# Kernel tuning notes

Measured on AMD Instinct MI355X. Metric: run time of the kernel, lower is better.

Reference implementation:

```python
import jax, jax.numpy as jnp
import numpy as np

L, R, H, E = 2, 3, 512, 32768

def setup_inputs() -> dict:
    key = jax.random.key(0)
    ks = jax.random.split(key, 8)
    s = 1.0 / np.sqrt(H)  # keep activations sane
    return {
        "v_repr": jax.random.normal(ks[0], (E, H), jnp.float32),
        "r_repr": jax.random.normal(ks[1], (E, H), jnp.float32),
        "ent_roles": jax.random.randint(ks[2], (E,), 0, R),
        "W": jax.random.normal(ks[3], (L, R, H, H), jnp.float32) * s,
        "W_b": jnp.zeros((L, R, H), jnp.float32),
        "U": jax.random.normal(ks[4], (L, R, H, H), jnp.float32) * s,
        "U_b": jnp.zeros((L, R, H), jnp.float32),
        "P1": jax.random.normal(ks[5], (L, R, H, H), jnp.float32) * s,
        "P1_b": jnp.zeros((L, R, H), jnp.float32),
        "P2": jax.random.normal(ks[6], (L, R, H, H), jnp.float32) * s,
        "P2_b": jnp.zeros((L, R, H), jnp.float32),
        "layer_idx": 0,
    }

def reference(v_repr, r_repr, ent_roles, W, W_b, U, U_b, P1, P1_b, P2, P2_b, layer_idx):
    # Select this layer's per-role weight stacks: (R, H, H) / (R, H)
    Wl, Wbl = W[layer_idx], W_b[layer_idx]
    Ul, Ubl = U[layer_idx], U_b[layer_idx]
    P1l, P1bl = P1[layer_idx], P1_b[layer_idx]
    P2l, P2bl = P2[layer_idx], P2_b[layer_idx]
    out = jnp.zeros_like(v_repr)
    for role in range(R):  # fixed small role set
        mask = (ent_roles == role)[:, None]  # (E, 1)
        v_p = v_repr @ Wl[role].T + Wbl[role]   # nn.Linear: x @ W.T + b
        r_p = r_repr @ Ul[role].T + Ubl[role]
        h = v_p * r_p
        p = jax.nn.relu(h @ P1l[role].T + P1bl[role]) @ P2l[role].T + P2bl[role]
        out = out + jnp.where(mask, p, 0.0)
    return out
```

## Files before the change

### kernel.cpp

```cpp
#include <hip/hip_runtime.h>
#include <cstdint>
#include <cstddef>

#define E_TOT 32768
#define HD    512
#define NR    3
#define EPAD_MAX 33152
#define NTM   259
#define NB    1036
#define NBS1  1036

typedef __attribute__((ext_vector_type(8))) short short8;
typedef __attribute__((ext_vector_type(4))) float f32x4;

static __device__ __forceinline__ unsigned short f2bf(float f) {
  union { float f; unsigned int u; } x; x.f = f;
  unsigned int u = x.u;
  return (unsigned short)((u + 0x7fffu + ((u >> 16) & 1u)) >> 16);
}
static __device__ __forceinline__ float bf2f(unsigned short h) {
  union { unsigned int u; float f; } x; x.u = ((unsigned int)h) << 16;
  return x.f;
}

static __device__ __forceinline__ void gload_lds16(const void* g, void* l) {
  __builtin_amdgcn_global_load_lds(
      (const __attribute__((address_space(1))) unsigned int*)g,
      (__attribute__((address_space(3))) unsigned int*)l, 16, 0, 0);
}

template <int NWG>
static __device__ __forceinline__ int chunk_swz(int bid) {
  constexpr int q = NWG / 8, r = NWG % 8;
  const int x = bid & 7, i = bid >> 3;
  return (x < r) ? x * (q + 1) + i : r * (q + 1) + (x - r) * q + i;
}


#define AL128(x) (((x) + 127) & ~127)

__global__ void k_sort1(const int* __restrict__ roles, int* __restrict__ ctrl) {
  __shared__ int cnt[NR];
  const int t = threadIdx.x;
  if (t < NR) cnt[t] = 0;
  __syncthreads();
  int c0 = 0, c1 = 0, c2 = 0;
  for (int i = t; i < E_TOT; i += 1024) {
    const int ro = roles[i];
    c0 += (ro == 0); c1 += (ro == 1); c2 += (ro == 2);
  }
  if (c0) atomicAdd(&cnt[0], c0);
  if (c1) atomicAdd(&cnt[1], c1);
  if (c2) atomicAdd(&cnt[2], c2);
  __syncthreads();
  if (t == 0) {
    const int off1 = AL128(cnt[0]);
    const int off2 = AL128(off1 + cnt[1]);
    const int ptot = AL128(off2 + cnt[2]);
    ctrl[0] = cnt[0]; ctrl[1] = cnt[1]; ctrl[2] = cnt[2];
    ctrl[4] = 0; ctrl[5] = off1; ctrl[6] = off2; ctrl[7] = ptot;
    ctrl[9] = 0; ctrl[10] = off1; ctrl[11] = off2;
  }
}

__global__ void k_scatter(const int* __restrict__ roles, int* __restrict__ ctrl,
                          int* __restrict__ perm) {
  int e = blockIdx.x * 256 + threadIdx.x;
  int lane = threadIdx.x & 63;
  int role = roles[e];
#pragma unroll
  for (int r = 0; r < NR; ++r) {
    unsigned long long m = __ballot(role == r);
    if (!m) continue;
    int leader = __ffsll((unsigned long long)m) - 1;
    int base = 0;
    if (lane == leader) base = atomicAdd(&ctrl[9 + r], (int)__popcll(m));
    base = __shfl(base, leader);
    if (role == r) {
      int rank = (int)__popcll(m & ((1ull << lane) - 1ull));
      perm[base + rank] = e;
    }
  }
}

__global__ void k_padfill(const int* __restrict__ ctrl, int* __restrict__ perm) {
#pragma unroll
  for (int r = 0; r < NR; ++r) {
    const int start = ctrl[4 + r] + ctrl[r];
    const int end = (r < 2) ? ctrl[5 + r] : EPAD_MAX;
    const int fill = (ctrl[r] > 0) ? perm[ctrl[4 + r]] : 0;
    for (int i = start + (int)threadIdx.x; i < end; i += 256) perm[i] = fill;
  }
}

__global__ void k_convw(const float* __restrict__ W, const float* __restrict__ U,
                        const float* __restrict__ P1, const float* __restrict__ P2,
                        const int* __restrict__ dlayer, short* __restrict__ dst) {
  const int per = NR * HD * HD;
  const int which = blockIdx.y;
  const float* src = (which == 0) ? W : (which == 1) ? U : (which == 2) ? P1 : P2;
  src += (size_t)dlayer[0] * per;
  short* d = dst + (size_t)which * per;
  int i = (blockIdx.x * 256 + threadIdx.x) * 4;
  if (i >= per) return;
  float4 v = *(const float4*)(src + i);
  short4 o;
  o.x = (short)f2bf(v.x); o.y = (short)f2bf(v.y);
  o.z = (short)f2bf(v.z); o.w = (short)f2bf(v.w);
  *(short4*)(d + i) = o;
}

__global__ __launch_bounds__(512) void k_s1(
    const float* __restrict__ vsrc, const float* __restrict__ rsrc,
    const short* __restrict__ B0, const short* __restrict__ B1,
    const float* __restrict__ bias0, const float* __restrict__ bias1,
    const int* __restrict__ dlayer, const int* __restrict__ ctrl,
    const int* __restrict__ perm, short* __restrict__ vp,
    short* __restrict__ rp) {
  __shared__ short As[128 * 64];
  __shared__ short Bs[256 * 64];

  int lb = chunk_swz<NBS1>(blockIdx.x);
  const int pair = lb >= (NTM * 2) ? 1 : 0;
  lb -= pair * (NTM * 2);
  const int m0 = (lb >> 1) * 128, n0 = (lb & 1) * 256;
  if (m0 >= ctrl[7]) return;
  const int role = (m0 >= ctrl[6]) ? 2 : (m0 >= ctrl[5] ? 1 : 0);

  const int tid = threadIdx.x;
  const int lane = tid & 63;
  const int wv = tid >> 6;
  const int wr = wv >> 2, wc = wv & 3;
  const int krow = lane & 15, ku = lane >> 4;

  const short* Brole = (pair ? B1 : B0) + (size_t)role * HD * HD;
  const float* Af32 = pair ? rsrc : vsrc;

  unsigned asrc[2];
#pragma unroll
  for (int j = 0; j < 2; ++j) {
    const int g = j * 512 + tid;
    const int row = g >> 3;
    const int ud = (g & 7) ^ (row & 7);
    asrc[j] = (unsigned)perm[m0 + row] * HD + ud * 8;
  }
  unsigned bsrc[4];
#pragma unroll
  for (int j = 0; j < 4; ++j) {
    const int g = j * 512 + tid;
    const int row = g >> 3;
    const int ud = (g & 7) ^ (row & 7);
    bsrc[j] = (unsigned)(n0 + row) * HD + ud * 8;
  }

  f32x4 acc[4][4];
#pragma unroll
  for (int a = 0; a < 4; ++a)
#pragma unroll
    for (int b = 0; b < 4; ++b) acc[a][b] = (f32x4)0.f;

  for (int t = 0; t < 8; ++t) {
    const int k0 = t * 64;
#pragma unroll
    for (int j = 0; j < 4; ++j)
      gload_lds16(Brole + (size_t)bsrc[j] + k0, &Bs[(j * 512 + tid) * 8]);
#pragma unroll
    for (int j = 0; j < 2; ++j) {
      const float* s = Af32 + (size_t)asrc[j] + k0;
      const float4 x0 = *(const float4*)s;
      const float4 x1 = *(const float4*)(s + 4);
      short8 o;
#pragma unroll
      for (int e = 0; e < 4; ++e) {
        o[e]     = (short)f2bf(((const float*)&x0)[e]);
        o[4 + e] = (short)f2bf(((const float*)&x1)[e]);
      }
      *(short8*)&As[(j * 512 + tid) * 8] = o;
    }
    __syncthreads();
    short8 fa[4][2], fb[4][2];
#pragma unroll
    for (int mi = 0; mi < 4; ++mi)
#pragma unroll
      for (int ks = 0; ks < 2; ++ks) {
        const int row = wr * 64 + mi * 16 + krow;
        fa[mi][ks] = *(const short8*)&As[row * 64 + (((ks * 4 + ku) ^ (row & 7)) * 8)];
      }
#pragma unroll
    for (int ni = 0; ni < 4; ++ni)
#pragma unroll
      for (int ks = 0; ks < 2; ++ks) {
        const int row = wc * 64 + ni * 16 + krow;
        fb[ni][ks] = *(const short8*)&Bs[row * 64 + (((ks * 4 + ku) ^ (row & 7)) * 8)];
      }
#pragma unroll
    for (int ks = 0; ks < 2; ++ks)
#pragma unroll
      for (int mi = 0; mi < 4; ++mi)
#pragma unroll
        for (int ni = 0; ni < 4; ++ni)
          acc[mi][ni] = __builtin_amdgcn_mfma_f32_16x16x32_bf16(
              fa[mi][ks], fb[ni][ks], acc[mi][ni], 0, 0, 0);
    __syncthreads();
  }

  const int ld = dlayer[0];
  const float* bias = (pair ? bias1 : bias0) + ((size_t)ld * NR + role) * HD + n0;
  short* outS = pair ? rp : vp;

#pragma unroll
  for (int ni = 0; ni < 4; ++ni) {
    const int col = wc * 64 + ni * 16 + krow;
    const float b = bias[col];
#pragma unroll
    for (int mi = 0; mi < 4; ++mi) {
      const int rbase = m0 + wr * 64 + mi * 16 + ku * 4;
#pragma unroll
      for (int j = 0; j < 4; ++j) {
        const float val = acc[mi][ni][j] + b;
        outS[(size_t)(rbase + j) * HD + n0 + col] = (short)f2bf(val);
      }
    }
  }
}

template <int AM, int OM>
__global__ __launch_bounds__(256) void k_mm(
    const short* __restrict__ A0, const short* __restrict__ A1,
    const short* __restrict__ B0, const float* __restrict__ bias0,
    const int* __restrict__ dlayer, const int* __restrict__ ctrl,
    const int* __restrict__ perm, short* __restrict__ outS,
    float* __restrict__ outF) {
  __shared__ short As[128 * 64];
  __shared__ short Bs[128 * 64];

  const int lb = chunk_swz<NB>(blockIdx.x);
  const int m0 = (lb >> 2) * 128, n0 = (lb & 3) * 128;
  if (m0 >= ctrl[7]) return;
  const int role = (m0 >= ctrl[6]) ? 2 : (m0 >= ctrl[5] ? 1 : 0);

  const int tid = threadIdx.x;
  const int lane = tid & 63;
  const int wv = tid >> 6;
  const int wr = wv >> 1, wc = wv & 1;
  const int krow = lane & 15, ku = lane >> 4;

  const short* Brole = B0 + (size_t)role * HD * HD;

  unsigned asrc[4], bsrc[4];
#pragma unroll
  for (int j = 0; j < 4; ++j) {
    const int g = j * 256 + tid;
    const int row = g >> 3;
    const int ud = (g & 7) ^ (row & 7);
    asrc[j] = (unsigned)(m0 + row) * HD + ud * 8;
    bsrc[j] = (unsigned)(n0 + row) * HD + ud * 8;
  }

  f32x4 acc[4][4];
#pragma unroll
  for (int a = 0; a < 4; ++a)
#pragma unroll
    for (int b = 0; b < 4; ++b) acc[a][b] = (f32x4)0.f;

  for (int t = 0; t < 8; ++t) {
    const int k0 = t * 64;
#pragma unroll
    for (int j = 0; j < 4; ++j)
      gload_lds16(Brole + (size_t)bsrc[j] + k0, &Bs[(j * 256 + tid) * 8]);
    if constexpr (AM == 0) {
#pragma unroll
      for (int j = 0; j < 4; ++j)
        gload_lds16(A0 + (size_t)asrc[j] + k0, &As[(j * 256 + tid) * 8]);
    } else {
#pragma unroll
      for (int j = 0; j < 4; ++j) {
        const short8 av = *(const short8*)(A0 + (size_t)asrc[j] + k0);
        const short8 ar = *(const short8*)(A1 + (size_t)asrc[j] + k0);
        short8 o;
#pragma unroll
        for (int e = 0; e < 8; ++e)
          o[e] = (short)f2bf(bf2f((unsigned short)av[e]) *
                             bf2f((unsigned short)ar[e]));
        *(short8*)&As[(j * 256 + tid) * 8] = o;
      }
    }
    __syncthreads();
    short8 fa[4][2], fb[4][2];
#pragma unroll
    for (int mi = 0; mi < 4; ++mi)
#pragma unroll
      for (int ks = 0; ks < 2; ++ks) {
        const int row = wr * 64 + mi * 16 + krow;
        fa[mi][ks] = *(const short8*)&As[row * 64 + (((ks * 4 + ku) ^ (row & 7)) * 8)];
      }
#pragma unroll
    for (int ni = 0; ni < 4; ++ni)
#pragma unroll
      for (int ks = 0; ks < 2; ++ks) {
        const int row = wc * 64 + ni * 16 + krow;
        fb[ni][ks] = *(const short8*)&Bs[row * 64 + (((ks * 4 + ku) ^ (row & 7)) * 8)];
      }
#pragma unroll
    for (int ks = 0; ks < 2; ++ks)
#pragma unroll
      for (int mi = 0; mi < 4; ++mi)
#pragma unroll
        for (int ni = 0; ni < 4; ++ni)
          acc[mi][ni] = __builtin_amdgcn_mfma_f32_16x16x32_bf16(
              fa[mi][ks], fb[ni][ks], acc[mi][ni], 0, 0, 0);
    __syncthreads();
  }

  const int ld = dlayer[0];
  const float* bias = bias0 + ((size_t)ld * NR + role) * HD + n0;

  int pg[4][4];
  if constexpr (OM == 2) {
#pragma unroll
    for (int mi = 0; mi < 4; ++mi)
#pragma unroll
      for (int j = 0; j < 4; ++j)
        pg[mi][j] = perm[m0 + wr * 64 + mi * 16 + ku * 4 + j];
  }

#pragma unroll
  for (int ni = 0; ni < 4; ++ni) {
    const int col = wc * 64 + ni * 16 + krow;
    const float b = bias[col];
#pragma unroll
    for (int mi = 0; mi < 4; ++mi) {
      const int rbase = m0 + wr * 64 + mi * 16 + ku * 4;
#pragma unroll
      for (int j = 0; j < 4; ++j) {
        float val = acc[mi][ni][j] + b;
        if constexpr (OM == 1) {
          val = fmaxf(val, 0.f);
          outS[(size_t)(rbase + j) * HD + n0 + col] = (short)f2bf(val);
        } else {
          outF[(size_t)pg[mi][j] * HD + n0 + col] = val;
        }
      }
    }
  }
}


extern "C" void kernel_launch(void* const* d_in, const int* in_sizes, int n_in,
                              void* d_out, int out_size, void* d_ws, size_t ws_size,
                              hipStream_t stream) {
  const float* v    = (const float*)d_in[0];
  const float* r    = (const float*)d_in[1];
  const int*   rol  = (const int*)d_in[2];
  const float* W    = (const float*)d_in[3];
  const float* Wb   = (const float*)d_in[4];
  const float* U    = (const float*)d_in[5];
  const float* Ub   = (const float*)d_in[6];
  const float* P1   = (const float*)d_in[7];
  const float* P1b  = (const float*)d_in[8];
  const float* P2   = (const float*)d_in[9];
  const float* P2b  = (const float*)d_in[10];
  const int*   dly  = (const int*)d_in[11];

  char* ws = (char*)d_ws;
  int* ctrl = (int*)ws;
  int* perm = (int*)(ws + 256);
  short* Wbf = (short*)(ws + 132864);
  short* Ubf  = Wbf + (size_t)NR * HD * HD;
  short* P1bf = Ubf + (size_t)NR * HD * HD;
  short* P2bf = P1bf + (size_t)NR * HD * HD;
  short* rp = (short*)(ws + 6424320);
  short* tb = rp + (size_t)EPAD_MAX * HD;
  short* vp  = (short*)d_out;
  float* out = (float*)d_out;

  k_sort1<<<1, 1024, 0, stream>>>(rol, ctrl);
  k_scatter<<<E_TOT / 256, 256, 0, stream>>>(rol, ctrl, perm);
  k_padfill<<<1, 256, 0, stream>>>(ctrl, perm);
  k_convw<<<dim3((NR * HD * HD) / 4 / 256, 4, 1), 256, 0, stream>>>(W, U, P1, P2, dly, Wbf);

  k_s1<<<NBS1, 512, 0, stream>>>(v, r, Wbf, Ubf, Wb, Ub, dly, ctrl, perm, vp, rp);
  k_mm<1, 1><<<NB, 256, 0, stream>>>(vp, rp, P1bf, P1b, dly, ctrl, perm, tb, nullptr);
  k_mm<0, 2><<<NB, 256, 0, stream>>>(tb, nullptr, P2bf, P2b, dly, ctrl, perm, nullptr, out);

  (void)in_sizes; (void)n_in; (void)out_size; (void)ws_size;
}
```

Baseline: 186.0 us.

## Double-buffer stage-1 GEMM with register prefetch and smaller 128x128 tiles

The first projection kernel (v@W, r@U) moves from 128x256 tiles to 128x128 tiles, which doubles the block count. It adds double-buffered LDS for A and B and prefetches the next K-slice's fp32 A into registers and B directly into LDS while the current slice runs MFMA. The fp32-to-bf16 conversion is deferred until after compute. This aims to hide global-load latency and raise parallelism, at the cost of more LDS per block, more register pressure, and less reuse of each B tile.

```diff
diff --git a/kernel.cpp b/kernel.cpp
--- a/kernel.cpp
+++ b/kernel.cpp
@@ -8,7 +8,7 @@
 #define EPAD_MAX 33152
 #define NTM   259
 #define NB    1036
-#define NBS1  1036
+#define NBS1  2072
 
 typedef __attribute__((ext_vector_type(8))) short short8;
 typedef __attribute__((ext_vector_type(4))) float f32x4;
@@ -117,91 +117,116 @@
     const int* __restrict__ dlayer, const int* __restrict__ ctrl,
     const int* __restrict__ perm, short* __restrict__ vp,
     short* __restrict__ rp) {
-  __shared__ short As[128 * 64];
-  __shared__ short Bs[256 * 64];
+  __shared__ short As[2][128 * 64];
+  __shared__ short Bs[2][128 * 64];
 
   int lb = chunk_swz<NBS1>(blockIdx.x);
-  const int pair = lb >= (NTM * 2) ? 1 : 0;
-  lb -= pair * (NTM * 2);
-  const int m0 = (lb >> 1) * 128, n0 = (lb & 1) * 256;
+  const int pair = lb >= NB ? 1 : 0;
+  lb -= pair * NB;
+  const int m0 = (lb >> 2) * 128, n0 = (lb & 3) * 128;
   if (m0 >= ctrl[7]) return;
   const int role = (m0 >= ctrl[6]) ? 2 : (m0 >= ctrl[5] ? 1 : 0);
 
   const int tid = threadIdx.x;
   const int lane = tid & 63;
   const int wv = tid >> 6;
-  const int wr = wv >> 2, wc = wv & 3;
+  const int wr = wv >> 1, wc = wv & 1;
   const int krow = lane & 15, ku = lane >> 4;
 
   const short* Brole = (pair ? B1 : B0) + (size_t)role * HD * HD;
   const float* Af32 = pair ? rsrc : vsrc;
 
   unsigned asrc[2];
+  unsigned bsrc[2];
 #pragma unroll
   for (int j = 0; j < 2; ++j) {
     const int g = j * 512 + tid;
     const int row = g >> 3;
     const int ud = (g & 7) ^ (row & 7);
     asrc[j] = (unsigned)perm[m0 + row] * HD + ud * 8;
-  }
-  unsigned bsrc[4];
-#pragma unroll
-  for (int j = 0; j < 4; ++j) {
-    const int g = j * 512 + tid;
-    const int row = g >> 3;
-    const int ud = (g & 7) ^ (row & 7);
     bsrc[j] = (unsigned)(n0 + row) * HD + ud * 8;
   }
 
-  f32x4 acc[4][4];
-#pragma unroll
-  for (int a = 0; a < 4; ++a)
+  f32x4 acc[2][4];
+#pragma unroll
+  for (int a = 0; a < 2; ++a)
 #pragma unroll
     for (int b = 0; b < 4; ++b) acc[a][b] = (f32x4)0.f;
 
+  float4 areg[2][2][2];
+
+#define LOADA(pp, K0)                                                          \
+  _Pragma("unroll") for (int j = 0; j < 2; ++j) {                              \
+    const float* s_ = Af32 + (size_t)asrc[j] + (K0);                           \
+    areg[pp][j][0] = *(const float4*)s_;                                       \
+    areg[pp][j][1] = *(const float4*)(s_ + 4);                                 \
+  }
+
+#define LOADB(bi, K0)                                                          \
+  _Pragma("unroll") for (int j = 0; j < 2; ++j)                                \
+    gload_lds16(Brole + (size_t)bsrc[j] + (K0), &Bs[bi][(j * 512 + tid) * 8]);
+
+#define CVTA(pp, bi)                                                           \
+  _Pragma("unroll") for (int j = 0; j < 2; ++j) {                              \
+    short8 o_;                                                                 \
+    _Pragma("unroll") for (int e = 0; e < 4; ++e) {                            \
+      o_[e]     = (short)f2bf(((const float*)&areg[pp][j][0])[e]);             \
+      o_[4 + e] = (short)f2bf(((const float*)&areg[pp][j][1])[e]);             \
+    }                                                                          \
+    *(short8*)&As[bi][(j * 512 + tid) * 8] = o_;                               \
+  }
+
+  LOADA(0, 0)
+  LOADB(0, 0)
+  asm volatile("s_waitcnt vmcnt(2)" ::: "memory");
+  CVTA(0, 0)
+  asm volatile("s_waitcnt vmcnt(0) lgkmcnt(0)" ::: "memory");
+  __builtin_amdgcn_s_barrier();
+  __builtin_amdgcn_sched_barrier(0);
+
   for (int t = 0; t < 8; ++t) {
-    const int k0 = t * 64;
-#pragma unroll
-    for (int j = 0; j < 4; ++j)
-      gload_lds16(Brole + (size_t)bsrc[j] + k0, &Bs[(j * 512 + tid) * 8]);
-#pragma unroll
-    for (int j = 0; j < 2; ++j) {
-      const float* s = Af32 + (size_t)asrc[j] + k0;
-      const float4 x0 = *(const float4*)s;
-      const float4 x1 = *(const float4*)(s + 4);
-      short8 o;
-#pragma unroll
-      for (int e = 0; e < 4; ++e) {
-        o[e]     = (short)f2bf(((const float*)&x0)[e]);
-        o[4 + e] = (short)f2bf(((const float*)&x1)[e]);
-      }
-      *(short8*)&As[(j * 512 + tid) * 8] = o;
-    }
-    __syncthreads();
-    short8 fa[4][2], fb[4][2];
-#pragma unroll
-    for (int mi = 0; mi < 4; ++mi)
+    const int cur = t & 1, nxt = cur ^ 1;
+    if (t < 7) {
+      LOADA(nxt, (t + 1) * 64)
+      LOADB(nxt, (t + 1) * 64)
+      asm volatile("s_waitcnt vmcnt(6)" ::: "memory");
+    } else {
+      asm volatile("s_waitcnt vmcnt(0)" ::: "memory");
+    }
+    __builtin_amdgcn_s_barrier();
+    __builtin_amdgcn_sched_barrier(0);
+
+    short8 fa[2][2], fb[4][2];
+#pragma unroll
+    for (int mi = 0; mi < 2; ++mi)
 #pragma unroll
       for (int ks = 0; ks < 2; ++ks) {
-        const int row = wr * 64 + mi * 16 + krow;
-        fa[mi][ks] = *(const short8*)&As[row * 64 + (((ks * 4 + ku) ^ (row & 7)) * 8)];
+        const int row = wr * 32 + mi * 16 + krow;
+        fa[mi][ks] = *(const short8*)&As[cur][row * 64 + (((ks * 4 + ku) ^ (row & 7)) * 8)];
       }
 #pragma unroll
     for (int ni = 0; ni < 4; ++ni)
 #pragma unroll
       for (int ks = 0; ks < 2; ++ks) {
         const int row = wc * 64 + ni * 16 + krow;
-        fb[ni][ks] = *(const short8*)&Bs[row * 64 + (((ks * 4 + ku) ^ (row & 7)) * 8)];
+        fb[ni][ks] = *(const short8*)&Bs[cur][row * 64 + (((ks * 4 + ku) ^ (row & 7)) * 8)];
       }
 #pragma unroll
     for (int ks = 0; ks < 2; ++ks)
 #pragma unroll
-      for (int mi = 0; mi < 4; ++mi)
+      for (int mi = 0; mi < 2; ++mi)
 #pragma unroll
         for (int ni = 0; ni < 4; ++ni)
           acc[mi][ni] = __builtin_amdgcn_mfma_f32_16x16x32_bf16(
               fa[mi][ks], fb[ni][ks], acc[mi][ni], 0, 0, 0);
-    __syncthreads();
+
+    if (t < 7) {
+      asm volatile("s_waitcnt vmcnt(2)" ::: "memory");
+      CVTA(nxt, nxt)
+    }
+    asm volatile("s_waitcnt lgkmcnt(0)" ::: "memory");
+    __builtin_amdgcn_s_barrier();
+    __builtin_amdgcn_sched_barrier(0);
   }
 
   const int ld = dlayer[0];
@@ -213,8 +238,8 @@
     const int col = wc * 64 + ni * 16 + krow;
     const float b = bias[col];
 #pragma unroll
-    for (int mi = 0; mi < 4; ++mi) {
-      const int rbase = m0 + wr * 64 + mi * 16 + ku * 4;
+    for (int mi = 0; mi < 2; ++mi) {
+      const int rbase = m0 + wr * 32 + mi * 16 + ku * 4;
 #pragma unroll
       for (int j = 0; j < 4; ++j) {
         const float val = acc[mi][ni][j] + b;
@@ -222,6 +247,9 @@
       }
     }
   }
+#undef LOADA
+#undef LOADB
+#undef CVTA
 }
 
 template <int AM, int OM>
```

New measurement: 197.0 us. 5.9% more time.
